# Performance work log

Hardware: AMD Instinct MI355X
Metric: run time of the kernel (lower is better)

## Reference

```python
import jax, jax.numpy as jnp
import numpy as np

B, T, FB, C = 2, 256, 128, 128
H_T, H_F, BAND = 4, 4, 16
INNER = 4 * C


def setup_inputs() -> dict:
    key = jax.random.key(0)
    ks = jax.random.split(key, 8)
    g = lambda k, shp: jax.random.normal(k, shp, jnp.float32) * 0.02
    return {
        "x": jax.random.normal(ks[0], (B, T, FB, C), jnp.float32),
        # temporal pre-norm + MHA (in_proj [3C,C], out_proj [C,C])
        "ln_t_w": jnp.ones((C,), jnp.float32), "ln_t_b": jnp.zeros((C,), jnp.float32),
        "t_wi": g(ks[1], (3 * C, C)), "t_bi": jnp.zeros((3 * C,), jnp.float32),
        "t_wo": g(ks[2], (C, C)), "t_bo": jnp.zeros((C,), jnp.float32),
        # frequency pre-norm + MHA
        "ln_f_w": jnp.ones((C,), jnp.float32), "ln_f_b": jnp.zeros((C,), jnp.float32),
        "f_wi": g(ks[3], (3 * C, C)), "f_bi": jnp.zeros((3 * C,), jnp.float32),
        "f_wo": g(ks[4], (C, C)), "f_bo": jnp.zeros((C,), jnp.float32),
        # FFN pre-norm + two linears
        "ln_n_w": jnp.ones((C,), jnp.float32), "ln_n_b": jnp.zeros((C,), jnp.float32),
        "w1": g(ks[5], (INNER, C)), "b1": jnp.zeros((INNER,), jnp.float32),
        "w2": g(ks[6], (C, INNER)), "b2": jnp.zeros((C,), jnp.float32),
    }


def _ln(x, w, b, eps=1e-5):
    mu = x.mean(-1, keepdims=True)
    var = ((x - mu) ** 2).mean(-1, keepdims=True)
    return (x - mu) * jax.lax.rsqrt(var + eps) * w + b


def _mha(x, wi, bi, wo, bo, h, mask):
    """torch.nn.MultiheadAttention equivalent. x: [..., S, C], mask: additive [S, S]."""
    c = x.shape[-1]
    dh = c // h
    qkv = x @ wi.T + bi
    q, k, v = jnp.split(qkv, 3, axis=-1)
    split = lambda t: t.reshape(t.shape[:-1] + (h, dh)).swapaxes(-2, -3)  # [..., h, S, dh]
    q, k, v = split(q), split(k), split(v)
    scores = jnp.einsum('...hqd,...hkd->...hqk', q, k) * (1.0 / np.sqrt(dh)) + mask
    attn = jax.nn.softmax(scores, axis=-1)
    o = jnp.einsum('...hqk,...hkd->...hqd', attn, v)
    o = o.swapaxes(-2, -3).reshape(x.shape)
    return o @ wo.T + bo


def _causal_mask(n):
    i = jnp.arange(n)
    return jnp.where(i[:, None] >= i[None, :], 0.0, -jnp.inf).astype(jnp.float32)


def _band_mask(n, band):
    i = jnp.arange(n)
    return jnp.where(jnp.abs(i[:, None] - i[None, :]) <= band, 0.0, -jnp.inf).astype(jnp.float32)


def reference(x, ln_t_w, ln_t_b, t_wi, t_bi, t_wo, t_bo,
              ln_f_w, ln_f_b, f_wi, f_bi, f_wo, f_bo,
              ln_n_w, ln_n_b, w1, b1, w2, b2):
    cm = _causal_mask(x.shape[1])      # [T, T]
    bm = _band_mask(x.shape[2], BAND)  # [F, F]
    # temporal causal MHSA per frequency bin (pre-norm residual)
    xt = _ln(x, ln_t_w, ln_t_b).transpose(0, 2, 1, 3)  # [B, F, T, C]
    x = x + _mha(xt, t_wi, t_bi, t_wo, t_bo, H_T, cm).transpose(0, 2, 1, 3)
    # banded local MHSA over frequency per time step
    xf = _ln(x, ln_f_w, ln_f_b)  # [B, T, F, C]
    x = x + _mha(xf, f_wi, f_bi, f_wo, f_bo, H_F, bm)
    # FFN (Linear -> exact GELU -> Linear)
    xn = _ln(x, ln_n_w, ln_n_b)
    h = jax.nn.gelu(xn @ w1.T + b1, approximate=False)
    x = x + (h @ w2.T + b2)
    return x
```

## Files before the change

### kernel.cpp

```cpp
#include <hip/hip_runtime.h>
#include <math.h>

typedef __bf16 bf16;
typedef __bf16 bf16x8 __attribute__((ext_vector_type(8)));
typedef __bf16 bf16x4 __attribute__((ext_vector_type(4)));
typedef __bf16 bf16x2 __attribute__((ext_vector_type(2)));
typedef float f32x4 __attribute__((ext_vector_type(4)));
typedef float f32x2 __attribute__((ext_vector_type(2)));
typedef float f32x16 __attribute__((ext_vector_type(16)));
typedef unsigned int u32;
typedef unsigned int u32x4 __attribute__((ext_vector_type(4)));

#define AS1 __attribute__((address_space(1)))
#define AS3 __attribute__((address_space(3)))

static __device__ __forceinline__ f32x4 mfma16(bf16x8 a, bf16x8 b, f32x4 c) {
    return __builtin_amdgcn_mfma_f32_16x16x32_bf16(a, b, c, 0, 0, 0);
}
static __device__ __forceinline__ f32x16 mfma32(bf16x8 a, bf16x8 b, f32x16 c) {
    return __builtin_amdgcn_mfma_f32_32x32x16_bf16(a, b, c, 0, 0, 0);
}
static __device__ __forceinline__ u32 pk2(float a, float b) {
    bf16x2 v; v[0] = (bf16)a; v[1] = (bf16)b;
    return __builtin_bit_cast(u32, v);
}
static __device__ __forceinline__ float gelu_f(float x) {
    float u = 0.7978845608f * x * __builtin_fmaf(0.044715f, x * x, 1.0f);
    float e = __expf(2.0f * u);
    return x - x * __builtin_amdgcn_rcpf(e + 1.0f);
}

__global__ __launch_bounds__(256) void cvt_w6(
    const float* __restrict__ s0, const float* __restrict__ s1,
    const float* __restrict__ s2, const float* __restrict__ s3,
    const float* __restrict__ s4, const float* __restrict__ s5,
    bf16* __restrict__ dst)
{
    int i = (blockIdx.x * 256 + threadIdx.x) * 4;
    const float* src; int off;
    if      (i <  49152) { src = s0; off = 0; }
    else if (i <  65536) { src = s1; off = 49152; }
    else if (i < 114688) { src = s2; off = 65536; }
    else if (i < 131072) { src = s3; off = 114688; }
    else if (i < 196608) { src = s4; off = 131072; }
    else                 { src = s5; off = 196608; }
    f32x4 v = *(const f32x4*)&src[i - off];
    bf16x4 b;
    b[0] = (bf16)v[0]; b[1] = (bf16)v[1]; b[2] = (bf16)v[2]; b[3] = (bf16)v[3];
    *(bf16x4*)&dst[i] = b;
}

template<int OUT_BF16, int RES, int RESBF, int GELU_, int LNA, int RMAP, int KT, int NT>
__global__ __launch_bounds__(256) void gemm_rw(
    const bf16* __restrict__ A, const bf16* __restrict__ W,
    const float* __restrict__ bias, const void* __restrict__ res,
    void* __restrict__ outp,
    const float* __restrict__ xf, const float* __restrict__ lnaw,
    const float* __restrict__ lnab)
{
    constexpr int N = NT * 128;
    __shared__ __align__(16) bf16 Bs[128 * 64];
    const int tid  = threadIdx.x;
    const int lane = tid & 63;
    const int w    = tid >> 6;
    const int li = lane & 15, g = lane >> 4;
    const int m0 = blockIdx.x * 64;
    const int arow = m0 + w * 16 + li;
    int srow = arow;
    if constexpr (RMAP) {
        int b = arow >> 15, t = (arow >> 7) & 255, f = arow & 127;
        srow = (b << 15) + (f << 8) + t;
    }
    const bf16* ap = A + (size_t)srow * KT;

    bf16x8 afrag[4];
    if constexpr (LNA) {
        int b = arow >> 15, f = (arow >> 8) & 127, t = arow & 255;
        const float* xp = xf + (((size_t)b * 256 + t) * 128 + f) * 128;
        f32x4 cv[8];
        #pragma unroll
        for (int cc = 0; cc < 4; ++cc) {
            cv[2 * cc]     = *(const f32x4*)&xp[cc * 32 + g * 8];
            cv[2 * cc + 1] = *(const f32x4*)&xp[cc * 32 + g * 8 + 4];
        }
        float sm = 0.f, sq = 0.f;
        #pragma unroll
        for (int i = 0; i < 8; ++i)
            #pragma unroll
            for (int j = 0; j < 4; ++j) { float v = cv[i][j]; sm += v; sq += v * v; }
        sm += __shfl_xor(sm, 16); sm += __shfl_xor(sm, 32);
        sq += __shfl_xor(sq, 16); sq += __shfl_xor(sq, 32);
        float mu = sm * 0.0078125f;
        float rs = rsqrtf(sq * 0.0078125f - mu * mu + 1e-5f);
        #pragma unroll
        for (int cc = 0; cc < 4; ++cc) {
            f32x4 w0 = *(const f32x4*)&lnaw[cc * 32 + g * 8];
            f32x4 w1 = *(const f32x4*)&lnaw[cc * 32 + g * 8 + 4];
            f32x4 b0 = *(const f32x4*)&lnab[cc * 32 + g * 8];
            f32x4 b1 = *(const f32x4*)&lnab[cc * 32 + g * 8 + 4];
            #pragma unroll
            for (int j = 0; j < 4; ++j) {
                afrag[cc][j]     = (bf16)((cv[2 * cc][j]     - mu) * rs * w0[j] + b0[j]);
                afrag[cc][4 + j] = (bf16)((cv[2 * cc + 1][j] - mu) * rs * w1[j] + b1[j]);
            }
        }
    } else if constexpr (KT == 128) {
        #pragma unroll
        for (int cc = 0; cc < 4; ++cc)
            afrag[cc] = *(const bf16x8*)&ap[cc * 32 + g * 8];
    }

    #pragma unroll
    for (int t = 0; t < NT; ++t) {
        const int n0 = t * 128;
        f32x4 acc[8] = {};

        #pragma unroll
        for (int k0 = 0; k0 < KT; k0 += 64) {
            #pragma unroll
            for (int it = 0; it < 4; ++it) {
                int idx = it * 256 + tid;
                int brow = idx >> 3, bch = idx & 7;
                const bf16* gp = W + (size_t)(n0 + brow) * KT + k0 + ((bch ^ (brow & 7)) * 8);
                __builtin_amdgcn_global_load_lds((AS1 void*)gp, (AS3 void*)(Bs + idx * 8), 16, 0, 0);
            }
            bf16x8 av0, av1;
            if constexpr (KT != 128) {
                av0 = *(const bf16x8*)&ap[k0 + g * 8];
                av1 = *(const bf16x8*)&ap[k0 + 32 + g * 8];
            }
            __syncthreads();
            #pragma unroll
            for (int kk = 0; kk < 2; ++kk) {
                bf16x8 av;
                if constexpr (KT == 128) av = afrag[(k0 >> 5) + kk];
                else                     av = kk ? av1 : av0;
                #pragma unroll
                for (int j = 0; j < 8; ++j) {
                    int brow = j * 16 + li;
                    int bch = (kk * 4 + g) ^ (li & 7);
                    bf16x8 bv = *(const bf16x8*)&Bs[brow * 64 + bch * 8];
                    acc[j] = mfma16(av, bv, acc[j]);
                }
            }
            __syncthreads();
        }

        float bcol[8];
        #pragma unroll
        for (int j = 0; j < 8; ++j) bcol[j] = bias[n0 + j * 16 + li];

        const int row0 = m0 + w * 16 + g * 4;
        #pragma unroll
        for (int r = 0; r < 4; ++r) {
            int row = row0 + r;
            #pragma unroll
            for (int j = 0; j < 8; ++j) {
                size_t off = (size_t)row * N + n0 + j * 16 + li;
                float v = acc[j][r] + bcol[j];
                if constexpr (RES) {
                    if constexpr (RESBF) v += (float)((const bf16*)res)[off];
                    else                 v += ((const float*)res)[off];
                }
                if constexpr (GELU_) v = gelu_f(v);
                if constexpr (OUT_BF16) ((bf16*)outp)[off] = (bf16)v;
                else                    ((float*)outp)[off] = v;
            }
        }
    }
}

__global__ __launch_bounds__(256) void ffn_fused(
    const bf16* __restrict__ A, const bf16* __restrict__ W1,
    const float* __restrict__ b1, const bf16* __restrict__ W2,
    const float* __restrict__ b2, const bf16* __restrict__ res,
    float* __restrict__ outp)
{
    __shared__ __align__(16) bf16 Bs[2][128 * 64];
    __shared__ __align__(16) bf16 hbuf[64 * 136];
    const int tid  = threadIdx.x;
    const int lane = tid & 63;
    const int w    = tid >> 6;
    const int li = lane & 15, g = lane >> 4;
    const int m0 = blockIdx.x * 64;
    const int arow = m0 + w * 16 + li;
    const bf16* ap = A + (size_t)arow * 128;

    bf16x8 axn[4];
    #pragma unroll
    for (int cc = 0; cc < 4; ++cc)
        axn[cc] = *(const bf16x8*)&ap[cc * 32 + g * 8];

    const int sidx  = tid;
    auto stageW1 = [&](int b, int t, int k0) {
        #pragma unroll
        for (int it = 0; it < 4; ++it) {
            int idx = it * 256 + sidx;
            int brow = idx >> 3, bch = idx & 7;
            const bf16* gp = W1 + (size_t)(t * 128 + brow) * 128 + k0 + ((bch ^ (brow & 7)) * 8);
            __builtin_amdgcn_global_load_lds((AS1 void*)gp, (AS3 void*)(Bs[b] + idx * 8), 16, 0, 0);
        }
    };
    auto stageW2 = [&](int b, int t, int k0) {
        #pragma unroll
        for (int it = 0; it < 4; ++it) {
            int idx = it * 256 + sidx;
            int brow = idx >> 3, bch = idx & 7;
            const bf16* gp = W2 + (size_t)brow * 512 + t * 128 + k0 + ((bch ^ (brow & 7)) * 8);
            __builtin_amdgcn_global_load_lds((AS1 void*)gp, (AS3 void*)(Bs[b] + idx * 8), 16, 0, 0);
        }
    };
    auto compute16 = [&](int b, bf16x8 av0, bf16x8 av1, f32x4* acc) {
        #pragma unroll
        for (int kk = 0; kk < 2; ++kk) {
            bf16x8 av = kk ? av1 : av0;
            #pragma unroll
            for (int j = 0; j < 8; ++j) {
                int brow = j * 16 + li;
                int bch = (kk * 4 + g) ^ (li & 7);
                bf16x8 bv = *(const bf16x8*)&Bs[b][brow * 64 + bch * 8];
                acc[j] = mfma16(av, bv, acc[j]);
            }
        }
    };

    f32x4 oacc[8] = {};

    stageW1(0, 0, 0);
    #pragma unroll
    for (int t = 0; t < 4; ++t) {
        f32x4 hacc[8] = {};

        __syncthreads();
        stageW1(1, t, 64);
        compute16(0, axn[0], axn[1], hacc);

        __syncthreads();
        stageW2(0, t, 0);
        compute16(1, axn[2], axn[3], hacc);

        float b1c[8];
        #pragma unroll
        for (int j = 0; j < 8; ++j) b1c[j] = b1[t * 128 + j * 16 + li];
        #pragma unroll
        for (int r = 0; r < 4; ++r) {
            int lrow = w * 16 + g * 4 + r;
            #pragma unroll
            for (int j = 0; j < 8; ++j)
                hbuf[lrow * 136 + j * 16 + li] = (bf16)gelu_f(hacc[j][r] + b1c[j]);
        }
        bf16x8 ah[4];
        #pragma unroll
        for (int cc = 0; cc < 4; ++cc)
            ah[cc] = *(const bf16x8*)&hbuf[(w * 16 + li) * 136 + cc * 32 + g * 8];

        __syncthreads();
        stageW2(1, t, 64);
        compute16(0, ah[0], ah[1], oacc);

        __syncthreads();
        if (t < 3) stageW1(0, t + 1, 0);
        compute16(1, ah[2], ah[3], oacc);
    }

    float b2c[8];
    #pragma unroll
    for (int j = 0; j < 8; ++j) b2c[j] = b2[j * 16 + li];
    const int row0 = m0 + w * 16 + g * 4;
    #pragma unroll
    for (int r = 0; r < 4; ++r) {
        int row = row0 + r;
        #pragma unroll
        for (int j = 0; j < 8; ++j) {
            size_t off = (size_t)row * 128 + j * 16 + li;
            outp[off] = oacc[j][r] + b2c[j] + (float)res[off];
        }
    }
}

template<int MODE, int RESBF>
__global__ __launch_bounds__(256) void attn_fused(
    const bf16* __restrict__ qkv, const bf16* __restrict__ Wo,
    const float* __restrict__ bo, const void* __restrict__ res,
    bf16* __restrict__ xc, bf16* __restrict__ xn,
    const float* __restrict__ lnw, const float* __restrict__ lnb)
{
    constexpr int S = (MODE == 0) ? 256 : 128;
    __shared__ __align__(16) char smem[2 * 20480 + 2048];
    float* red = (float*)(smem + 40960);
    const int tid = threadIdx.x;
    const int lane = tid & 63;
    const int w = tid >> 6;
    const int hi = lane >> 5;
    const int q31 = lane & 31;
    const int s = blockIdx.x;
    const int qb = blockIdx.y * 64;

    const size_t base = (size_t)s * S * 384;
    const bf16* qp = qkv + base + w * 32;

    const float sc = 0.17677669529663687f;
    bf16x8 qA0, qA1, qB0, qB1;
    {
        bf16x8 r0 = *(const bf16x8*)&qp[(size_t)(qb + q31) * 384 + hi * 8];
        bf16x8 r1 = *(const bf16x8*)&qp[(size_t)(qb + q31) * 384 + 16 + hi * 8];
        bf16x8 r2 = *(const bf16x8*)&qp[(size_t)(qb + 32 + q31) * 384 + hi * 8];
        bf16x8 r3 = *(const bf16x8*)&qp[(size_t)(qb + 32 + q31) * 384 + 16 + hi * 8];
        #pragma unroll
        for (int e = 0; e < 8; ++e) {
            qA0[e] = (bf16)((float)r0[e] * sc);
            qA1[e] = (bf16)((float)r1[e] * sc);
            qB0[e] = (bf16)((float)r2[e] * sc);
            qB1[e] = (bf16)((float)r3[e] * sc);
        }
    }

    f32x16 OA = {}, OB = {};
    float lA = 0.f, lB = 0.f;

    int klo, khi;
    if constexpr (MODE == 0) { klo = 0; khi = qb + 64; }
    else {
        klo = (qb > 16 ? (qb - 16) : 0) & ~31;
        khi = (qb + 80 < S) ? (qb + 80) : S;
    }

    const int seg = tid & 15, rw = tid >> 4;
    const char* qc = (const char*)qkv + base * 2;
    const int wdst = (seg >> 2) * 2560 + rw * 80 + (seg & 3) * 16;

    u32x4 rk0, rk1, rv0, rv1;
    auto gload = [&](int k0) {
        const char* r0 = qc + (size_t)(k0 + rw) * 768;
        const char* r1 = qc + (size_t)(k0 + rw + 16) * 768;
        rk0 = *(const u32x4*)(r0 + 256 + seg * 16);
        rk1 = *(const u32x4*)(r1 + 256 + seg * 16);
        rv0 = *(const u32x4*)(r0 + 512 + seg * 16);
        rv1 = *(const u32x4*)(r1 + 512 + seg * 16);
    };
    auto swrite = [&](char* buf) {
        *(u32x4*)(buf + wdst)                = rk0;
        *(u32x4*)(buf + wdst + 1280)         = rk1;
        *(u32x4*)(buf + 10240 + wdst)        = rv0;
        *(u32x4*)(buf + 10240 + wdst + 1280) = rv1;
    };

    gload(klo);
    swrite(smem);
    __syncthreads();
    int cur = 0;

    for (int k0 = klo; k0 < khi; k0 += 32) {
        bool notlast = (k0 + 32 < khi);
        if (notlast) gload(k0 + 32);

        char* buf = smem + cur * 20480;
        const char* kb = buf + w * 2560 + q31 * 80 + hi * 16;
        bf16x8 kf0 = *(const bf16x8*)(kb);
        bf16x8 kf1 = *(const bf16x8*)(kb + 32);
        const bf16* vb = (const bf16*)(buf + 10240) + w * 1280 + hi * 320 + q31;
        bf16x8 vf1, vf2;
        #pragma unroll
        for (int e = 0; e < 8; ++e) {
            vf1[e] = vb[e * 40];
            vf2[e] = vb[640 + e * 40];
        }

        auto step = [&](f32x16& O, float& l, bf16x8 q0, bf16x8 q1,
                        int qrow, bool doMask) {
            f32x16 st = {};
            st = mfma32(kf0, q0, st);
            st = mfma32(kf1, q1, st);
            if (doMask) {
                #pragma unroll
                for (int r = 0; r < 16; ++r) {
                    int krow = k0 + (r & 3) + 8 * (r >> 2) + 4 * hi;
                    bool ok;
                    if constexpr (MODE == 0) ok = (krow <= qrow);
                    else { int d = krow - qrow; ok = (d <= 16 && d >= -16); }
                    st[r] = ok ? st[r] : -3.0e38f;
                }
            }
            float ps = 0.f;
            #pragma unroll
            for (int r = 0; r < 16; ++r) {
                float p = __expf(st[r]);
                st[r] = p;
                ps += p;
            }
            ps += __shfl_xor(ps, 32);
            l += ps;

            u32 c01 = pk2(st[0], st[1]),   c23 = pk2(st[2], st[3]);
            u32 c45 = pk2(st[4], st[5]),   c67 = pk2(st[6], st[7]);
            u32 c89 = pk2(st[8], st[9]),   cAB = pk2(st[10], st[11]);
            u32 cCD = pk2(st[12], st[13]), cEF = pk2(st[14], st[15]);
            u32 x01 = __shfl_xor((int)c01, 32), x23 = __shfl_xor((int)c23, 32);
            u32 x45 = __shfl_xor((int)c45, 32), x67 = __shfl_xor((int)c67, 32);
            u32 x89 = __shfl_xor((int)c89, 32), xAB = __shfl_xor((int)cAB, 32);
            u32 xCD = __shfl_xor((int)cCD, 32), xEF = __shfl_xor((int)cEF, 32);
            u32x4 b1w = hi ? u32x4{x45, x67, c45, c67} : u32x4{c01, c23, x01, x23};
            u32x4 b2w = hi ? u32x4{xCD, xEF, cCD, cEF} : u32x4{c89, cAB, x89, xAB};
            bf16x8 B1 = __builtin_bit_cast(bf16x8, b1w);
            bf16x8 B2 = __builtin_bit_cast(bf16x8, b2w);

            O = mfma32(vf1, B1, O);
            O = mfma32(vf2, B2, O);
        };

        bool actA, actB, dgA, dgB;
        if constexpr (MODE == 0) {
            actA = (k0 <= qb); actB = true;
            dgA = (k0 == qb);  dgB = (k0 == qb + 32);
        } else {
            actA = (k0 >= qb - 47) && (k0 <= qb + 47);
            actB = (k0 >= qb - 15) && (k0 <= qb + 79);
            dgA = true; dgB = true;
        }
        if (actA) step(OA, lA, qA0, qA1, qb + q31, dgA);
        if (actB) step(OB, lB, qB0, qB1, qb + 32 + q31, dgB);

        if (notlast) swrite(smem + (cur ^ 1) * 20480);
        __syncthreads();
        cur ^= 1;
    }

    bf16* o_lds = (bf16*)smem;
    float invA = 1.f / lA, invB = 1.f / lB;
    #pragma unroll
    for (int mb = 0; mb < 4; ++mb) {
        bf16x4 ovA, ovB;
        #pragma unroll
        for (int j = 0; j < 4; ++j) {
            ovA[j] = (bf16)(OA[mb * 4 + j] * invA);
            ovB[j] = (bf16)(OB[mb * 4 + j] * invB);
        }
        *(bf16x4*)&o_lds[q31 * 136 + w * 32 + mb * 8 + hi * 4] = ovA;
        *(bf16x4*)&o_lds[(32 + q31) * 136 + w * 32 + mb * 8 + hi * 4] = ovB;
    }
    __syncthreads();

    const int li = lane & 15, g = lane >> 4;
    bf16x8 af[4][4];
    #pragma unroll
    for (int mi = 0; mi < 4; ++mi)
        #pragma unroll
        for (int kk = 0; kk < 4; ++kk)
            af[mi][kk] = *(const bf16x8*)&o_lds[(mi * 16 + li) * 136 + kk * 32 + g * 8];

    f32x4 acc[4][2] = {};
    #pragma unroll
    for (int ni = 0; ni < 2; ++ni) {
        #pragma unroll
        for (int kk = 0; kk < 4; ++kk) {
            bf16x8 bv = *(const bf16x8*)&Wo[(size_t)(w * 32 + ni * 16 + li) * 128 + kk * 32 + g * 8];
            #pragma unroll
            for (int mi = 0; mi < 4; ++mi)
                acc[mi][ni] = mfma16(af[mi][kk], bv, acc[mi][ni]);
        }
    }

    float vals[4][2][4];
    #pragma unroll
    for (int mi = 0; mi < 4; ++mi) {
        #pragma unroll
        for (int r = 0; r < 4; ++r) {
            int lrl = mi * 16 + g * 4 + r;
            int grow = qb + lrl;
            size_t rrow;
            if constexpr (MODE == 0) {
                int b = s >> 7, f = s & 127;
                rrow = ((size_t)(b * 256 + grow)) * 128 + f;
            } else {
                int b = s >> 8, t = s & 255;
                rrow = (size_t)b * 32768 + (size_t)grow * 256 + t;
            }
            #pragma unroll
            for (int ni = 0; ni < 2; ++ni) {
                int col = w * 32 + ni * 16 + li;
                float v = acc[mi][ni][r] + bo[col];
                if constexpr (RESBF) v += (float)((const bf16*)res)[rrow * 128 + col];
                else                 v += ((const float*)res)[rrow * 128 + col];
                vals[mi][ni][r] = v;
            }
        }
    }
    #pragma unroll
    for (int mi = 0; mi < 4; ++mi) {
        #pragma unroll
        for (int r = 0; r < 4; ++r) {
            float sm = vals[mi][0][r] + vals[mi][1][r];
            float sq = vals[mi][0][r] * vals[mi][0][r] + vals[mi][1][r] * vals[mi][1][r];
            #pragma unroll
            for (int off = 1; off < 16; off <<= 1) {
                sm += __shfl_xor(sm, off);
                sq += __shfl_xor(sq, off);
            }
            if (li == 0) {
                red[(mi * 16 + g * 4 + r) * 8 + w * 2 + 0] = sm;
                red[(mi * 16 + g * 4 + r) * 8 + w * 2 + 1] = sq;
            }
        }
    }
    __syncthreads();
    #pragma unroll
    for (int mi = 0; mi < 4; ++mi) {
        #pragma unroll
        for (int r = 0; r < 4; ++r) {
            int mrow = mi * 16 + g * 4 + r;
            f32x4 p0 = *(const f32x4*)&red[mrow * 8 + 0];
            f32x4 p1 = *(const f32x4*)&red[mrow * 8 + 4];
            float smt = p0[0] + p0[2] + p1[0] + p1[2];
            float sqt = p0[1] + p0[3] + p1[1] + p1[3];
            float mu = smt * 0.0078125f;
            float rs = rsqrtf(sqt * 0.0078125f - mu * mu + 1e-5f);
            size_t woff = ((size_t)s * S + qb + mrow) * 128;
            #pragma unroll
            for (int ni = 0; ni < 2; ++ni) {
                int col = w * 32 + ni * 16 + li;
                float v = vals[mi][ni][r];
                xc[woff + col] = (bf16)v;
                xn[woff + col] = (bf16)((v - mu) * rs * lnw[col] + lnb[col]);
            }
        }
    }
}

extern "C" void kernel_launch(void* const* d_in, const int* in_sizes, int n_in,
                              void* d_out, int out_size, void* d_ws, size_t ws_size,
                              hipStream_t stream) {
    const float* x      = (const float*)d_in[0];
    const float* ln_t_w = (const float*)d_in[1];
    const float* ln_t_b = (const float*)d_in[2];
    const float* t_wi   = (const float*)d_in[3];
    const float* t_bi   = (const float*)d_in[4];
    const float* t_wo   = (const float*)d_in[5];
    const float* t_bo   = (const float*)d_in[6];
    const float* ln_f_w = (const float*)d_in[7];
    const float* ln_f_b = (const float*)d_in[8];
    const float* f_wi   = (const float*)d_in[9];
    const float* f_bi   = (const float*)d_in[10];
    const float* f_wo   = (const float*)d_in[11];
    const float* f_bo   = (const float*)d_in[12];
    const float* ln_n_w = (const float*)d_in[13];
    const float* ln_n_b = (const float*)d_in[14];
    const float* w1     = (const float*)d_in[15];
    const float* b1     = (const float*)d_in[16];
    const float* w2     = (const float*)d_in[17];
    const float* b2     = (const float*)d_in[18];

    char* ws = (char*)d_ws;
    bf16* wbf  = (bf16*)ws;
    bf16* xn   = (bf16*)(ws + 524288);
    bf16* qkvh = (bf16*)(ws + 524288 + 16777216);
    bf16* xcA  = (bf16*)(ws + 524288 + 16777216 + 67108864 + 16777216);
    bf16* xcB  = (bf16*)(ws + 524288 + 16777216 + 67108864 + 2 * 16777216);
    float* out = (float*)d_out;

    const bf16* twi_b = wbf + 0;
    const bf16* two_b = wbf + 49152;
    const bf16* fwi_b = wbf + 65536;
    const bf16* fwo_b = wbf + 114688;
    const bf16* w1_b  = wbf + 131072;
    const bf16* w2_b  = wbf + 196608;

    cvt_w6<<<256, 256, 0, stream>>>(t_wi, t_wo, f_wi, f_wo, w1, w2, wbf);

    gemm_rw<1, 0, 0, 0, 1, 0, 128, 3><<<1024, 256, 0, stream>>>(
        nullptr, twi_b, t_bi, nullptr, qkvh, x, ln_t_w, ln_t_b);
    attn_fused<0, 0><<<dim3(256, 4), 256, 0, stream>>>(
        qkvh, two_b, t_bo, x, xcA, xn, ln_f_w, ln_f_b);

    gemm_rw<1, 0, 0, 0, 0, 1, 128, 3><<<1024, 256, 0, stream>>>(
        xn, fwi_b, f_bi, nullptr, qkvh, nullptr, nullptr, nullptr);
    attn_fused<1, 1><<<dim3(512, 2), 256, 0, stream>>>(
        qkvh, fwo_b, f_bo, xcA, xcB, xn, ln_n_w, ln_n_b);

    ffn_fused<<<1024, 256, 0, stream>>>(xn, w1_b, b1, w2_b, b2, xcB, out);

    (void)in_sizes; (void)n_in; (void)out_size; (void)ws_size;
}
```

Baseline: 158.4 us.

## Prefetch two weight stages ahead in FFN kernel with vmcnt-based waits

The FFN kernel now keeps two weight tile loads in flight. It waits with s_waitcnt vmcnt(4) plus raw s_barrier instead of __syncthreads, which drains all outstanding loads. Each buffer is refilled right after the compute that consumed it, so global-to-LDS copies overlap more with MFMA work. The risk is that correctness depends on exact per-thread load counts and on barrier placement relative to the hbuf staging.

```diff
diff --git a/kernel.cpp b/kernel.cpp
--- a/kernel.cpp
+++ b/kernel.cpp
@@ -191,11 +191,10 @@
     for (int cc = 0; cc < 4; ++cc)
         axn[cc] = *(const bf16x8*)&ap[cc * 32 + g * 8];
 
-    const int sidx  = tid;
     auto stageW1 = [&](int b, int t, int k0) {
         #pragma unroll
         for (int it = 0; it < 4; ++it) {
-            int idx = it * 256 + sidx;
+            int idx = it * 256 + tid;
             int brow = idx >> 3, bch = idx & 7;
             const bf16* gp = W1 + (size_t)(t * 128 + brow) * 128 + k0 + ((bch ^ (brow & 7)) * 8);
             __builtin_amdgcn_global_load_lds((AS1 void*)gp, (AS3 void*)(Bs[b] + idx * 8), 16, 0, 0);
@@ -204,7 +203,7 @@
     auto stageW2 = [&](int b, int t, int k0) {
         #pragma unroll
         for (int it = 0; it < 4; ++it) {
-            int idx = it * 256 + sidx;
+            int idx = it * 256 + tid;
             int brow = idx >> 3, bch = idx & 7;
             const bf16* gp = W2 + (size_t)brow * 512 + t * 128 + k0 + ((bch ^ (brow & 7)) * 8);
             __builtin_amdgcn_global_load_lds((AS1 void*)gp, (AS3 void*)(Bs[b] + idx * 8), 16, 0, 0);
@@ -227,17 +226,27 @@
     f32x4 oacc[8] = {};
 
     stageW1(0, 0, 0);
+    stageW1(1, 0, 64);
+
     #pragma unroll
     for (int t = 0; t < 4; ++t) {
         f32x4 hacc[8] = {};
 
-        __syncthreads();
-        stageW1(1, t, 64);
+        asm volatile("s_waitcnt vmcnt(4)" ::: "memory");
+        __builtin_amdgcn_s_barrier();
+        __builtin_amdgcn_sched_barrier(0);
         compute16(0, axn[0], axn[1], hacc);
-
-        __syncthreads();
+        __builtin_amdgcn_sched_barrier(0);
+        __builtin_amdgcn_s_barrier();
         stageW2(0, t, 0);
+
+        asm volatile("s_waitcnt vmcnt(4)" ::: "memory");
+        __builtin_amdgcn_s_barrier();
+        __builtin_amdgcn_sched_barrier(0);
         compute16(1, axn[2], axn[3], hacc);
+        __builtin_amdgcn_sched_barrier(0);
+        __builtin_amdgcn_s_barrier();
+        stageW2(1, t, 64);
 
         float b1c[8];
         #pragma unroll
@@ -254,13 +263,22 @@
         for (int cc = 0; cc < 4; ++cc)
             ah[cc] = *(const bf16x8*)&hbuf[(w * 16 + li) * 136 + cc * 32 + g * 8];
 
-        __syncthreads();
-        stageW2(1, t, 64);
+        asm volatile("s_waitcnt vmcnt(4)" ::: "memory");
+        __builtin_amdgcn_s_barrier();
+        __builtin_amdgcn_sched_barrier(0);
         compute16(0, ah[0], ah[1], oacc);
-
-        __syncthreads();
+        __builtin_amdgcn_sched_barrier(0);
+        __builtin_amdgcn_s_barrier();
         if (t < 3) stageW1(0, t + 1, 0);
+
+        if (t < 3) asm volatile("s_waitcnt vmcnt(4)" ::: "memory");
+        else       asm volatile("s_waitcnt vmcnt(0)" ::: "memory");
+        __builtin_amdgcn_s_barrier();
+        __builtin_amdgcn_sched_barrier(0);
         compute16(1, ah[2], ah[3], oacc);
+        __builtin_amdgcn_sched_barrier(0);
+        __builtin_amdgcn_s_barrier();
+        if (t < 3) stageW1(1, t + 1, 64);
     }
 
     float b2c[8];
```

After: 148.1 us. -6.5%, faster.
